# Optimization experiments

Measured on AMD Instinct MI355X. Metric: run time of the kernel, lower is better.

The kernel has to match this reference:

```python
import jax, jax.numpy as jnp
import numpy as np

B, D = 4096, 1024
TEMPERATURE = 0.07


def setup_inputs() -> dict:
    key = jax.random.key(0)
    k1, k2, k3, k4, k5, k6 = jax.random.split(key, 6)
    return {
        "mri_features": jax.random.normal(k1, (B, D), dtype=jnp.float32),
        "pet_features": jax.random.normal(k2, (B, D), dtype=jnp.float32),
        "labels": jax.random.randint(k3, (B,), 0, 3, dtype=jnp.int64),
        "subtype_mri": jax.random.randint(k4, (B,), 0, 4, dtype=jnp.int64),
        "subtype_pet": jax.random.randint(k5, (B,), 0, 4, dtype=jnp.int64),
        "clinical_similarity": jax.random.uniform(k6, (B, B), dtype=jnp.float32),
    }


def _build_weights(labels, subtype_mri, subtype_pet, clinical_similarity):
    # vectorized form of the O(B^2) python loop
    same_label = labels[:, None] == labels[None, :]
    label_zero = labels[:, None] == 0
    sub_match = (subtype_mri[:, None] == subtype_mri[None, :]) & (
        subtype_pet[:, None] == subtype_pet[None, :]
    )
    n = labels.shape[0]
    not_diag = ~jnp.eye(n, dtype=bool)
    mask = same_label & (label_zero | sub_match) & not_diag
    weights = jnp.where(mask, clinical_similarity, 0.0)
    row_sums = weights.sum(axis=1, keepdims=True)
    row_sums = jnp.where(row_sums == 0, 1.0, row_sums)
    return weights / row_sums


def _contrastive(fi, fj, weights):
    fi = fi / jnp.linalg.norm(fi, axis=1, keepdims=True)
    fj = fj / jnp.linalg.norm(fj, axis=1, keepdims=True)
    sim = jnp.matmul(fi, fj.T) / TEMPERATURE  # [B, B]
    log_sm = jax.nn.log_softmax(sim, axis=1)
    return -jnp.sum(weights * log_sm) / fi.shape[0]


def reference(mri_features, pet_features, labels, subtype_mri, subtype_pet, clinical_similarity):
    weights = _build_weights(labels, subtype_mri, subtype_pet, clinical_similarity)
    pairs = [
        (mri_features, pet_features),
        (pet_features, mri_features),
        (mri_features, mri_features),
        (pet_features, pet_features),
    ]
    total = 0.0
    for fi, fj in pairs:
        total = total + _contrastive(fi, fj, weights)
    return total / len(pairs)
```

## Files before the change

kernel.cpp:

```cpp
#include <hip/hip_runtime.h>
#include <hip/hip_bf16.h>
#include <math.h>

typedef __attribute__((ext_vector_type(8))) short bf16x8;
typedef __attribute__((ext_vector_type(4))) short bf16x4;
typedef __attribute__((ext_vector_type(4))) float f32x4;

#define NB 4096
#define ND 1024
#define INV_T 14.2857142857142857f

__device__ inline unsigned short f2bf(float x) {
    __hip_bfloat16 h = __float2bfloat16(x);
    return *reinterpret_cast<unsigned short*>(&h);
}
__device__ inline float bf2f(unsigned short u) {
    unsigned v = ((unsigned)u) << 16;
    return __uint_as_float(v);
}
__device__ inline void gload16(const void* g, void* l) {
    __builtin_amdgcn_global_load_lds(
        (const __attribute__((address_space(1))) void*)g,
        (__attribute__((address_space(3))) void*)l, 16, 0, 0);
}

__global__ __launch_bounds__(256) void norm_kernel(
        const float* __restrict__ M, const float* __restrict__ P,
        __hip_bfloat16* __restrict__ Mn, __hip_bfloat16* __restrict__ Pn) {
    int row = blockIdx.x & (NB - 1);
    const float* src = (blockIdx.x < NB) ? M : P;
    __hip_bfloat16* dst = (blockIdx.x < NB) ? Mn : Pn;
    int tid = threadIdx.x;
    float4 v = ((const float4*)(src + (size_t)row * ND))[tid];
    float ss = v.x * v.x + v.y * v.y + v.z * v.z + v.w * v.w;
    for (int off = 32; off; off >>= 1) ss += __shfl_down(ss, off);
    __shared__ float red[4];
    int lane = tid & 63, w = tid >> 6;
    if (lane == 0) red[w] = ss;
    __syncthreads();
    float rn = rsqrtf(red[0] + red[1] + red[2] + red[3]);
    ushort4 o;
    o.x = f2bf(v.x * rn); o.y = f2bf(v.y * rn);
    o.z = f2bf(v.z * rn); o.w = f2bf(v.w * rn);
    *(ushort4*)((unsigned short*)dst + (size_t)row * ND + tid * 4) = o;
}

__global__ __launch_bounds__(256) void key_kernel(
        const int* __restrict__ labels, const int* __restrict__ sm,
        const int* __restrict__ sp, int* __restrict__ code) {
    int i = blockIdx.x * 256 + threadIdx.x;
    if (i < NB) {
        int l = labels[i];
        code[i] = (l == 0) ? 0x40000000 : (1 + l + (sm[i] << 8) + (sp[i] << 16));
    }
}

__global__ __launch_bounds__(256) void rowsumw_kernel(
        const float* __restrict__ cs, const int* __restrict__ code,
        unsigned short* __restrict__ W, float* __restrict__ flag) {
    int i = blockIdx.x;
    int ci = code[i];
    int tid = threadIdx.x;
    const float4* row = (const float4*)(cs + (size_t)i * NB);
    const int4* c4 = (const int4*)code;
    float4 v[4];
    int4 cj[4];
    float s = 0.f;
#pragma unroll
    for (int k = 0; k < 4; ++k) {
        int t = tid + k * 256;
        v[k] = row[t];
        cj[k] = c4[t];
        int j = t * 4;
        if (cj[k].x == ci && j + 0 != i) s += v[k].x;
        if (cj[k].y == ci && j + 1 != i) s += v[k].y;
        if (cj[k].z == ci && j + 2 != i) s += v[k].z;
        if (cj[k].w == ci && j + 3 != i) s += v[k].w;
    }
    for (int off = 1; off < 64; off <<= 1) s += __shfl_xor(s, off);
    __shared__ float red[4];
    int lane = tid & 63, w = tid >> 6;
    if (lane == 0) red[w] = s;
    __syncthreads();
    float tot = red[0] + red[1] + red[2] + red[3];
    float inv = (tot > 0.f) ? 1.f / tot : 0.f;
#pragma unroll
    for (int k = 0; k < 4; ++k) {
        int t = tid + k * 256;
        int j = t * 4;
        ushort4 o;
        o.x = (cj[k].x == ci && j + 0 != i) ? f2bf(v[k].x * inv) : (unsigned short)0;
        o.y = (cj[k].y == ci && j + 1 != i) ? f2bf(v[k].y * inv) : (unsigned short)0;
        o.z = (cj[k].z == ci && j + 2 != i) ? f2bf(v[k].z * inv) : (unsigned short)0;
        o.w = (cj[k].w == ci && j + 3 != i) ? f2bf(v[k].w * inv) : (unsigned short)0;
        *(ushort4*)&W[(size_t)i * NB + j] = o;
    }
    if (tid == 0) flag[i] = (tot > 0.f) ? 1.f : 0.f;
}

__global__ __launch_bounds__(256) void symw_kernel(unsigned short* __restrict__ W) {
    __shared__ unsigned short Ta[64][72], Tb[64][72];
    int b = blockIdx.x;
    int ti = 0, t = b;
    while (t >= 64 - ti) { t -= 64 - ti; ++ti; }
    int tj = ti + t;
    size_t ra = (size_t)ti * 64, rb = (size_t)tj * 64;
    int tid = threadIdx.x;
    int r = tid >> 2, c0 = (tid & 3) * 16;
    int4 a0 = *(const int4*)&W[(ra + r) * NB + rb + c0];
    int4 a1 = *(const int4*)&W[(ra + r) * NB + rb + c0 + 8];
    int4 b0 = *(const int4*)&W[(rb + r) * NB + ra + c0];
    int4 b1 = *(const int4*)&W[(rb + r) * NB + ra + c0 + 8];
    *(int4*)&Ta[r][c0] = a0;  *(int4*)&Ta[r][c0 + 8] = a1;
    *(int4*)&Tb[r][c0] = b0;  *(int4*)&Tb[r][c0 + 8] = b1;
    __syncthreads();
    unsigned short oa[16], ob[16];
#pragma unroll
    for (int c = 0; c < 16; ++c) {
        int cc = c0 + c;
        oa[c] = f2bf(bf2f(Ta[r][cc]) + bf2f(Tb[cc][r]));
        ob[c] = f2bf(bf2f(Tb[r][cc]) + bf2f(Ta[cc][r]));
    }
    *(int4*)&W[(ra + r) * NB + rb + c0]     = *(int4*)&oa[0];
    *(int4*)&W[(ra + r) * NB + rb + c0 + 8] = *(int4*)&oa[8];
    *(int4*)&W[(rb + r) * NB + ra + c0]     = *(int4*)&ob[0];
    *(int4*)&W[(rb + r) * NB + ra + c0 + 8] = *(int4*)&ob[8];
}

__global__ __launch_bounds__(512) void mega_gemm(
        const __hip_bfloat16* __restrict__ Mn, const __hip_bfloat16* __restrict__ Pn,
        const unsigned short* __restrict__ Wg,
        float* __restrict__ rowsum1, float* __restrict__ colsum1,
        float* __restrict__ rowsum3, float* __restrict__ rowsum4,
        float* __restrict__ dots) {
    __shared__ char smem[98304] __attribute__((aligned(16)));

    int tid = threadIdx.x;
    int lane = tid & 63, w = tid >> 6;
    int wm = w >> 1, wn = w & 1;
    int lr = lane & 15, lg = lane >> 4;

    int b = (blockIdx.x & 7) * 132 + (blockIdx.x >> 3);
    int bi, bj, ch, mode;
    const __hip_bfloat16 *A, *Bm;
    if (b < 512) {
        bi = b >> 5;
        bj = (b & 31) >> 1;
        ch = b & 1;
        A = Mn; Bm = Pn; mode = 0;
    } else {
        int s = b - 512;
        int md = (s >= 272) ? 1 : 0;
        s -= md * 272;
        ch = s & 1;
        int t = s >> 1;
        bi = 0;
        while (t >= 16 - bi) { t -= 16 - bi; ++bi; }
        bj = bi + t;
        A = md ? Pn : Mn; Bm = A;
        mode = 1 + md;
    }
    bool offdiag = (bi != bj);
    size_t rowBase = (size_t)bi * 256;
    size_t colBase = (size_t)bj * 256 + ch * 128;
    float* rowTgt = (mode == 0) ? rowsum1 : ((mode == 1) ? rowsum3 : rowsum4);
    float* colTgt = (mode == 0) ? colsum1 : rowTgt;

    int r16 = lane >> 2;
    int sch = ((lane & 3) ^ ((lane >> 3) & 3)) * 8;
    const __hip_bfloat16* gA = A + (rowBase + w * 32 + r16) * ND + sch;
    const __hip_bfloat16* gB = Bm + (colBase + w * 16 + r16) * ND + sch;

    f32x4 acc[4][4] = {};

#define STAGE(bufi, t) {                                                    \
        int k0_ = (t) * 32;                                                 \
        char* baseA_ = smem + (bufi) * 24576;                               \
        char* baseB_ = baseA_ + 16384;                                      \
        gload16(gA + k0_,           baseA_ + (w * 2    ) * 1024);           \
        gload16(gA + 16 * ND + k0_, baseA_ + (w * 2 + 1) * 1024);           \
        gload16(gB + k0_,           baseB_ + w * 1024);                     \
    }
#define COMPUTE(bufi) {                                                     \
        const __hip_bfloat16* sA = (const __hip_bfloat16*)(smem + (bufi) * 24576); \
        const __hip_bfloat16* sB = sA + 8192;                               \
        int cp = (lg ^ ((lr >> 1) & 3)) * 8;                                \
        bf16x8 av[4], bv[4];                                                \
        _Pragma("unroll")                                                   \
        for (int n = 0; n < 4; ++n)                                         \
            bv[n] = *(const bf16x8*)&sB[(wn * 64 + n * 16 + lr) * 32 + cp]; \
        _Pragma("unroll")                                                   \
        for (int i = 0; i < 4; ++i)                                         \
            av[i] = *(const bf16x8*)&sA[(wm * 64 + i * 16 + lr) * 32 + cp]; \
        _Pragma("unroll")                                                   \
        for (int i = 0; i < 4; ++i)                                         \
            _Pragma("unroll")                                               \
            for (int n = 0; n < 4; ++n)                                     \
                acc[i][n] = __builtin_amdgcn_mfma_f32_16x16x32_bf16(        \
                    av[i], bv[n], acc[i][n], 0, 0, 0);                      \
    }
#define BAR __builtin_amdgcn_s_barrier()

    STAGE(0, 0); STAGE(1, 1); STAGE(2, 2);
    asm volatile("s_waitcnt vmcnt(6)" ::: "memory"); BAR;
    for (int t = 0; t < 29; ++t) {
        STAGE((t + 3) & 3, t + 3);
        COMPUTE(t & 3);
        asm volatile("s_waitcnt vmcnt(6)" ::: "memory"); BAR;
    }
    COMPUTE(29 & 3);
    asm volatile("s_waitcnt vmcnt(3)" ::: "memory"); BAR;
    COMPUTE(30 & 3);
    asm volatile("s_waitcnt vmcnt(0)" ::: "memory"); BAR;
    COMPUTE(31 & 3);
    __syncthreads();
#undef STAGE
#undef COMPUTE
#undef BAR

    unsigned short* wl = (unsigned short*)smem;
    float d1 = 0.f;
    float cexp[4] = {0.f, 0.f, 0.f, 0.f};

#pragma unroll
    for (int c = 0; c < 8; ++c) {
        int q = w * 8 + c;
        int sr = 4 * q + (lane >> 4);
        int gchunk = (lane & 15) ^ (sr & 7);
        gload16(Wg + (rowBase + sr) * (size_t)NB + colBase + gchunk * 8,
                smem + q * 1024);
    }
    __syncthreads();
#pragma unroll
    for (int m = 0; m < 4; ++m) {
        float rexp[4] = {0.f, 0.f, 0.f, 0.f};
#pragma unroll
        for (int n = 0; n < 4; ++n) {
            int jl = wn * 64 + n * 16 + lr;
#pragma unroll
            for (int r = 0; r < 4; ++r) {
                int rl = wm * 64 + m * 16 + lg * 4 + r;
                float sim = acc[m][n][r] * INV_T;
                float e = __expf(sim - INV_T);
                rexp[r] += e;
                cexp[n] += e;
                int ck = (jl >> 3) ^ (rl & 7);
                d1 += bf2f(wl[rl * 128 + ck * 8 + (jl & 7)]) * sim;
            }
        }
#pragma unroll
        for (int r = 0; r < 4; ++r) {
            float v = rexp[r];
            v += __shfl_xor(v, 1); v += __shfl_xor(v, 2);
            v += __shfl_xor(v, 4); v += __shfl_xor(v, 8);
            if (lr == 0)
                atomicAdd(&rowTgt[rowBase + wm * 64 + m * 16 + lg * 4 + r], v);
        }
    }

    if (mode == 0 || offdiag) {
#pragma unroll
        for (int n = 0; n < 4; ++n) {
            float v = cexp[n];
            v += __shfl_xor(v, 16); v += __shfl_xor(v, 32);
            if (lg == 0)
                atomicAdd(&colTgt[colBase + wn * 64 + n * 16 + lr], v);
        }
    }

    float dtot = (mode != 0 && !offdiag) ? 0.5f * d1 : d1;
    for (int off = 32; off; off >>= 1) dtot += __shfl_xor(dtot, off);
    if (lane == 0) {
        if (mode == 0) atomicAdd(&dots[0], dtot);
        else           atomicAdd(&dots[1 + mode], dtot);
    }
}

__global__ __launch_bounds__(256) void finalize_kernel(
        const float* __restrict__ rowsum1, const float* __restrict__ colsum1,
        const float* __restrict__ rowsum3, const float* __restrict__ rowsum4,
        const float* __restrict__ flag, const float* __restrict__ dots,
        float* __restrict__ out) {
    int tid = threadIdx.x;
    float l = 0.f;
    for (int i = tid; i < NB; i += 256) {
        if (flag[i] != 0.f) {
            l += 4.f * INV_T + logf(rowsum1[i]) + logf(colsum1[i]) +
                 logf(rowsum3[i]) + logf(rowsum4[i]);
        }
    }
    for (int off = 32; off; off >>= 1) l += __shfl_down(l, off);
    __shared__ float red[4];
    int lane = tid & 63, w = tid >> 6;
    if (lane == 0) red[w] = l;
    __syncthreads();
    if (tid == 0) {
        float L = red[0] + red[1] + red[2] + red[3];
        float dt = dots[0] + dots[1] + dots[2] + dots[3];
        out[0] = (L - dt) / (4.0f * (float)NB);
    }
}

extern "C" void kernel_launch(void* const* d_in, const int* in_sizes, int n_in,
                              void* d_out, int out_size, void* d_ws, size_t ws_size,
                              hipStream_t stream) {
    const float* M = (const float*)d_in[0];
    const float* P = (const float*)d_in[1];
    const int* labels = (const int*)d_in[2];
    const int* sm = (const int*)d_in[3];
    const int* sp = (const int*)d_in[4];
    const float* cs = (const float*)d_in[5];
    float* out = (float*)d_out;

    char* ws = (char*)d_ws;
    __hip_bfloat16* Mn = (__hip_bfloat16*)ws;
    __hip_bfloat16* Pn = (__hip_bfloat16*)(ws + (size_t)8 * 1024 * 1024);
    unsigned short* W = (unsigned short*)(ws + (size_t)16 * 1024 * 1024);
    char* p = ws + (size_t)48 * 1024 * 1024;
    int* code = (int*)p;        p += 16384;
    float* flag = (float*)p;    p += 16384;
    float* rowsum1 = (float*)p; p += 16384;
    float* colsum1 = (float*)p; p += 16384;
    float* rowsum3 = (float*)p; p += 16384;
    float* rowsum4 = (float*)p; p += 16384;
    float* dots = (float*)p;

    hipMemsetAsync(rowsum1, 0, 4 * 16384 + 256, stream);

    norm_kernel<<<2 * NB, 256, 0, stream>>>(M, P, Mn, Pn);
    key_kernel<<<NB / 256, 256, 0, stream>>>(labels, sm, sp, code);
    rowsumw_kernel<<<NB, 256, 0, stream>>>(cs, code, W, flag);
    symw_kernel<<<2080, 256, 0, stream>>>(W);

    mega_gemm<<<1056, 512, 0, stream>>>(Mn, Pn, W, rowsum1, colsum1,
                                        rowsum3, rowsum4, dots);

    finalize_kernel<<<1, 256, 0, stream>>>(rowsum1, colsum1, rowsum3, rowsum4,
                                           flag, dots, out);
}
```

Measured before the change: 227.5 us.

## Double the K tile to 64 and switch to a 3-stage LDS pipeline

Each main-loop stage now loads a K-slice of 64 instead of 32, with a new 8-chunk XOR swizzle, and issues two MFMA k-steps per stage. Pipelining goes from 4 buffers of 24KB to 3 buffers of 48KB, so 16 stages run instead of 32. The aim is to halve the barriers and waitcnt points and amortize loop overhead per MFMA. In exchange, LDS use rises to 144KB, which limits occupancy to one block per CU and leaves fewer stages in flight.

```diff
diff --git a/kernel.cpp b/kernel.cpp
--- a/kernel.cpp
+++ b/kernel.cpp
@@ -133,7 +133,7 @@
         float* __restrict__ rowsum1, float* __restrict__ colsum1,
         float* __restrict__ rowsum3, float* __restrict__ rowsum4,
         float* __restrict__ dots) {
-    __shared__ char smem[98304] __attribute__((aligned(16)));
+    __shared__ char smem[147456] __attribute__((aligned(16)));
 
     int tid = threadIdx.x;
     int lane = tid & 63, w = tid >> 6;
@@ -166,53 +166,57 @@
     float* rowTgt = (mode == 0) ? rowsum1 : ((mode == 1) ? rowsum3 : rowsum4);
     float* colTgt = (mode == 0) ? colsum1 : rowTgt;
 
-    int r16 = lane >> 2;
-    int sch = ((lane & 3) ^ ((lane >> 3) & 3)) * 8;
-    const __hip_bfloat16* gA = A + (rowBase + w * 32 + r16) * ND + sch;
-    const __hip_bfloat16* gB = Bm + (colBase + w * 16 + r16) * ND + sch;
+    int sr8 = lane >> 3;
+    int sch = ((lane & 7) ^ sr8) * 8;
+    const __hip_bfloat16* gA = A + (rowBase + w * 32 + sr8) * ND + sch;
+    const __hip_bfloat16* gB = Bm + (colBase + w * 16 + sr8) * ND + sch;
 
     f32x4 acc[4][4] = {};
 
 #define STAGE(bufi, t) {                                                    \
-        int k0_ = (t) * 32;                                                 \
-        char* baseA_ = smem + (bufi) * 24576;                               \
-        char* baseB_ = baseA_ + 16384;                                      \
-        gload16(gA + k0_,           baseA_ + (w * 2    ) * 1024);           \
-        gload16(gA + 16 * ND + k0_, baseA_ + (w * 2 + 1) * 1024);           \
-        gload16(gB + k0_,           baseB_ + w * 1024);                     \
+        int k0_ = (t) * 64;                                                 \
+        char* baseA_ = smem + (bufi) * 49152;                               \
+        char* baseB_ = baseA_ + 32768;                                      \
+        _Pragma("unroll")                                                   \
+        for (int c = 0; c < 4; ++c)                                         \
+            gload16(gA + (size_t)c * 8 * ND + k0_, baseA_ + (w * 4 + c) * 1024); \
+        _Pragma("unroll")                                                   \
+        for (int c = 0; c < 2; ++c)                                         \
+            gload16(gB + (size_t)c * 8 * ND + k0_, baseB_ + (w * 2 + c) * 1024); \
     }
 #define COMPUTE(bufi) {                                                     \
-        const __hip_bfloat16* sA = (const __hip_bfloat16*)(smem + (bufi) * 24576); \
-        const __hip_bfloat16* sB = sA + 8192;                               \
-        int cp = (lg ^ ((lr >> 1) & 3)) * 8;                                \
-        bf16x8 av[4], bv[4];                                                \
+        const __hip_bfloat16* sA = (const __hip_bfloat16*)(smem + (bufi) * 49152); \
+        const __hip_bfloat16* sB = sA + 16384;                              \
         _Pragma("unroll")                                                   \
-        for (int n = 0; n < 4; ++n)                                         \
-            bv[n] = *(const bf16x8*)&sB[(wn * 64 + n * 16 + lr) * 32 + cp]; \
-        _Pragma("unroll")                                                   \
-        for (int i = 0; i < 4; ++i)                                         \
-            av[i] = *(const bf16x8*)&sA[(wm * 64 + i * 16 + lr) * 32 + cp]; \
-        _Pragma("unroll")                                                   \
-        for (int i = 0; i < 4; ++i)                                         \
+        for (int ks = 0; ks < 2; ++ks) {                                    \
+            int cp = ((ks * 4 + lg) ^ (lr & 7)) * 8;                        \
+            bf16x8 av[4], bv[4];                                            \
             _Pragma("unroll")                                               \
             for (int n = 0; n < 4; ++n)                                     \
-                acc[i][n] = __builtin_amdgcn_mfma_f32_16x16x32_bf16(        \
-                    av[i], bv[n], acc[i][n], 0, 0, 0);                      \
+                bv[n] = *(const bf16x8*)&sB[(wn * 64 + n * 16 + lr) * 64 + cp]; \
+            _Pragma("unroll")                                               \
+            for (int i = 0; i < 4; ++i)                                     \
+                av[i] = *(const bf16x8*)&sA[(wm * 64 + i * 16 + lr) * 64 + cp]; \
+            _Pragma("unroll")                                               \
+            for (int i = 0; i < 4; ++i)                                     \
+                _Pragma("unroll")                                           \
+                for (int n = 0; n < 4; ++n)                                 \
+                    acc[i][n] = __builtin_amdgcn_mfma_f32_16x16x32_bf16(    \
+                        av[i], bv[n], acc[i][n], 0, 0, 0);                  \
+        }                                                                   \
     }
 #define BAR __builtin_amdgcn_s_barrier()
 
-    STAGE(0, 0); STAGE(1, 1); STAGE(2, 2);
+    STAGE(0, 0); STAGE(1, 1);
     asm volatile("s_waitcnt vmcnt(6)" ::: "memory"); BAR;
-    for (int t = 0; t < 29; ++t) {
-        STAGE((t + 3) & 3, t + 3);
-        COMPUTE(t & 3);
+    for (int t = 0; t < 14; ++t) {
+        STAGE((t + 2) % 3, t + 2);
+        COMPUTE(t % 3);
         asm volatile("s_waitcnt vmcnt(6)" ::: "memory"); BAR;
     }
-    COMPUTE(29 & 3);
-    asm volatile("s_waitcnt vmcnt(3)" ::: "memory"); BAR;
-    COMPUTE(30 & 3);
+    COMPUTE(14 % 3);
     asm volatile("s_waitcnt vmcnt(0)" ::: "memory"); BAR;
-    COMPUTE(31 & 3);
+    COMPUTE(15 % 3);
     __syncthreads();
 #undef STAGE
 #undef COMPUTE
```

Result: slower. 233.6 us (+2.7%).
